# Kernel optimization log

Hardware: AMD Instinct MI355X
Metric: run time of the kernel (lower is better)

Reference implementation:

```python
import jax, jax.numpy as jnp
import numpy as np

BS, NS, NCP, NH, C, HID, R = 8, 2048, 8, 8, 128, 128, 128


def rotation_6d_to_matrix(d6):
    a1, a2 = d6[..., :3], d6[..., 3:]
    b1 = a1 / jnp.linalg.norm(a1, axis=-1, keepdims=True)
    b2 = a2 - jnp.sum(b1 * a2, axis=-1, keepdims=True) * b1
    b2 = b2 / jnp.linalg.norm(b2, axis=-1, keepdims=True)
    b3 = jnp.cross(b1, b2)
    return jnp.stack([b1, b2, b3], axis=-2)  # (..., 3, 3), rows b1,b2,b3


def _sample_plane(plane, uv):
    # plane: (B,C,R,R); uv: (B,N,2) in [0,1]; uv[...,0]->width, uv[...,1]->height
    Rr = plane.shape[-1]
    x = jnp.clip(uv[..., 0], 0.0, 1.0) * (Rr - 1)
    y = jnp.clip(uv[..., 1], 0.0, 1.0) * (Rr - 1)
    x0 = jnp.floor(x); y0 = jnp.floor(y)
    wx = x - x0; wy = y - y0
    x0i = x0.astype(jnp.int32); y0i = y0.astype(jnp.int32)
    x1i = jnp.minimum(x0i + 1, Rr - 1); y1i = jnp.minimum(y0i + 1, Rr - 1)
    gb = jax.vmap(lambda p, yi, xi: p[:, yi, xi])  # per-batch gather -> (C,N)
    f00 = gb(plane, y0i, x0i); f01 = gb(plane, y0i, x1i)
    f10 = gb(plane, y1i, x0i); f11 = gb(plane, y1i, x1i)
    wx = wx[:, None, :]; wy = wy[:, None, :]
    f = f00 * (1 - wx) * (1 - wy) + f01 * wx * (1 - wy) + f10 * (1 - wx) * wy + f11 * wx * wy
    return jnp.transpose(f, (0, 2, 1))  # (B,N,C)


def triplane_sample(p, pxz, pxy, pyz):
    # p: (B,N,3) in [0,1]^3; sum of bilinear samples from the three planes
    return (_sample_plane(pxz, p[..., jnp.array([0, 2])])
            + _sample_plane(pxy, p[..., jnp.array([0, 1])])
            + _sample_plane(pyz, p[..., jnp.array([1, 2])]))


def setup_inputs() -> dict:
    key = jax.random.key(0)
    ks = jax.random.split(key, 10)
    s = 1.0 / np.sqrt(C)
    return {
        "query_pos": jax.random.uniform(ks[0], (BS, NS, 9), dtype=jnp.float32),
        "plane_xz": jax.random.normal(ks[1], (BS, C, R, R), dtype=jnp.float32),
        "plane_xy": jax.random.normal(ks[2], (BS, C, R, R), dtype=jnp.float32),
        "plane_yz": jax.random.normal(ks[3], (BS, C, R, R), dtype=jnp.float32),
        "control_points": jax.random.normal(ks[4], (NCP, 3), dtype=jnp.float32) * 0.05,
        "W_v": jax.random.normal(ks[5], (C, HID), dtype=jnp.float32) * s,
        "b_v": jnp.zeros((HID,), jnp.float32),
        "W_w": jax.random.normal(ks[6], (C, NCP * NH), dtype=jnp.float32) * s,
        "b_w": jnp.zeros((NCP * NH,), jnp.float32),
        "W_o": jax.random.normal(ks[7], (HID, C), dtype=jnp.float32) * s,
        "b_o": jnp.zeros((C,), jnp.float32),
    }


def reference(query_pos, plane_xz, plane_xy, plane_yz, control_points,
              W_v, b_v, W_w, b_w, W_o, b_o):
    bs, ns, _ = query_pos.shape
    q_ori = query_pos[..., 3:]
    q_pos = query_pos[..., :3]
    feature = triplane_sample(q_pos, plane_xz, plane_xy, plane_yz)  # (bs,ns,C)
    rot = rotation_6d_to_matrix(q_ori)  # (bs,ns,3,3)
    # rotate control points: einsum('bnpd,bngd->bngp') with cp broadcast over (bs,ns)
    cp = jnp.einsum('bnpd,gd->bngp', rot, control_points)  # (bs,ns,ncp,3)
    anchor = q_pos[:, :, None, :] + cp  # (bs,ns,ncp,3)
    sf = triplane_sample(anchor.reshape(bs, ns * NCP, 3), plane_xz, plane_xy, plane_yz)
    sf = sf.reshape(bs * ns, NCP, C)  # head dim in torch code is a pure repeat
    feat = feature.reshape(bs * ns, C)
    w = (feat @ W_w + b_w).reshape(bs * ns, NCP, NH)  # (B,ncp,heads)
    vbase = sf @ W_v + b_v  # (B,ncp,hid); identical across repeated head dim
    # torch: (v * weights).sum((1,2)) with v_t[b,i,j,k]=vbase[b,j,k], w[b,i,j]
    out = jnp.einsum('bjk,bij->bk', vbase, w)  # (B,hid)
    out = out @ W_o + b_o
    out = out + feat
    return out.reshape(bs, ns, -1)
```

## Files before the change

### kernel.cpp

```cpp
#include <hip/hip_runtime.h>
#include <hip/hip_fp16.h>
#include <math.h>

constexpr int BS  = 8;
constexpr int NS  = 2048;
constexpr int NCP = 8;
constexpr int NH  = 8;
constexpr int C   = 128;
constexpr int HID = 128;
constexpr int RR  = 128;

constexpr int QPB = 8;
constexpr int VEC = 4;

constexpr int NPOS = RR * RR;
constexpr size_t PLE = (size_t)BS * NPOS * C;

constexpr int NBLK_T = 1536;
constexpr int QPOS   = 512;
constexpr int SPOS   = 256;
constexpr int LROWH  = 260;

constexpr int NBINS  = 4096;
constexpr int NQ     = BS * NS;

using f4v = __attribute__((ext_vector_type(4))) float;

struct F4 { float x, y, z, w; };
__device__ __forceinline__ F4 f4add(F4 a, F4 b) {
    return F4{a.x + b.x, a.y + b.y, a.z + b.z, a.w + b.w};
}
__device__ __forceinline__ F4 f4fma(F4 acc, float s, F4 v) {
    return F4{fmaf(s, v.x, acc.x), fmaf(s, v.y, acc.y),
              fmaf(s, v.z, acc.z), fmaf(s, v.w, acc.w)};
}

__global__ __launch_bounds__(256) void trans_prep_k(
    const float* __restrict__ pxz, const float* __restrict__ pxy,
    const float* __restrict__ pyz, __half* __restrict__ dst,
    const float* __restrict__ Wv, const float* __restrict__ bv,
    const float* __restrict__ Ww, const float* __restrict__ bw,
    const float* __restrict__ Wo,
    float* __restrict__ Wf, float* __restrict__ bf,
    float* __restrict__ Ww2, float* __restrict__ bw2,
    unsigned* __restrict__ hist)
{
    __shared__ __half lh[64 * LROWH];

    const int bid = blockIdx.x;
    const int t   = threadIdx.x;

    if (bid >= NBLK_T + 130) {
        hist[(bid - (NBLK_T + 130)) * 256 + t] = 0u;
        return;
    }
    if (bid >= NBLK_T) {
        const int k = bid - NBLK_T;
        const int c = t;
        if (c >= 128) return;
        if (k < 128) {
            float acc = 0.f;
            #pragma unroll 8
            for (int j = 0; j < 128; ++j) acc += Wv[k * 128 + j] * Wo[j * 128 + c];
            Wf[k * 128 + c] = acc;
        } else if (k == 128) {
            float acc = 0.f;
            #pragma unroll 8
            for (int j = 0; j < 128; ++j) acc += bv[j] * Wo[j * 128 + c];
            bf[c] = acc;
        } else {
            float s[NH];
            #pragma unroll
            for (int h = 0; h < NH; ++h) s[h] = 0.f;
            #pragma unroll
            for (int i = 0; i < NCP; ++i)
                #pragma unroll
                for (int h = 0; h < NH; ++h) s[h] += Ww[c * (NCP * NH) + i * NH + h];
            #pragma unroll
            for (int h = 0; h < NH; ++h) Ww2[c * NH + h] = s[h];
            if (c < NH) {
                float tt = 0.f;
                #pragma unroll
                for (int i = 0; i < NCP; ++i) tt += bw[i * NH + c];
                bw2[c] = tt;
            }
        }
        return;
    }

    const int b    = bid & 7;
    const int rem  = bid >> 3;
    const int pl   = rem >> 6;
    const int r2   = rem & 63;
    const int cg   = r2 >> 5;
    const int q    = r2 & 31;
    const int ch0  = cg * 64;
    const int pos0 = q * QPOS;

    const float* src = (pl == 0 ? pxz : (pl == 1 ? pxy : pyz))
                       + (size_t)b * C * NPOS;
    __half* d = dst + (size_t)(pl * BS + b) * ((size_t)NPOS * C);

    const int g32  = t >> 5;
    const int l32  = t & 31;

    f4v v[16];
    #pragma unroll
    for (int i = 0; i < 16; ++i) {
        const int chL  = g32 * 8 + (i >> 1);
        const int posL = ((i & 1) << 7) + (l32 << 2);
        v[i] = __builtin_nontemporal_load(reinterpret_cast<const f4v*>(
                   src + (size_t)(ch0 + chL) * NPOS + pos0 + posL));
    }

    #pragma unroll
    for (int sc = 0; sc < 2; ++sc) {
        __syncthreads();

        #pragma unroll
        for (int i = 0; i < 16; ++i) {
            const int chL  = g32 * 8 + (i >> 1);
            const int posL = ((i & 1) << 7) + (l32 << 2);
            __half2 h0 = __floats2half2_rn(v[i][0], v[i][1]);
            __half2 h1 = __floats2half2_rn(v[i][2], v[i][3]);
            uint2 w;
            w.x = *reinterpret_cast<unsigned*>(&h0);
            w.y = *reinterpret_cast<unsigned*>(&h1);
            *reinterpret_cast<uint2*>(&lh[chL * LROWH + posL]) = w;
        }

        f4v nv[16];
        if (sc < 1) {
            #pragma unroll
            for (int i = 0; i < 16; ++i) {
                const int chL  = g32 * 8 + (i >> 1);
                const int posL = ((i & 1) << 7) + (l32 << 2);
                nv[i] = __builtin_nontemporal_load(reinterpret_cast<const f4v*>(
                            src + (size_t)(ch0 + chL) * NPOS + pos0
                                + (sc + 1) * SPOS + posL));
            }
        }
        __syncthreads();

        const int cbase = (t & 7) * 8;
        #pragma unroll
        for (int j = 0; j < 8; ++j) {
            const int p = 32 * j + (t >> 3);
            unsigned w[4];
            #pragma unroll
            for (int k = 0; k < 4; ++k) {
                const unsigned lo = *reinterpret_cast<const unsigned short*>(
                                        &lh[(cbase + 2 * k) * LROWH + p]);
                const unsigned hi = *reinterpret_cast<const unsigned short*>(
                                        &lh[(cbase + 2 * k + 1) * LROWH + p]);
                w[k] = lo | (hi << 16);
            }
            *reinterpret_cast<uint4*>(
                d + (size_t)(pos0 + sc * SPOS + p) * C + ch0 + cbase) =
                make_uint4(w[0], w[1], w[2], w[3]);
        }

        #pragma unroll
        for (int i = 0; i < 16; ++i) v[i] = nv[i];
    }
}

__device__ __forceinline__ int bin_of(const float* qp) {
    int bx = min((int)(fminf(fmaxf(qp[0], 0.f), 1.f) * 8.f), 7);
    int by = min((int)(fminf(fmaxf(qp[1], 0.f), 1.f) * 8.f), 7);
    int bz = min((int)(fminf(fmaxf(qp[2], 0.f), 1.f) * 8.f), 7);
    int m = 0;
    #pragma unroll
    for (int i = 0; i < 3; ++i)
        m |= (((bx >> i) & 1) << (3 * i))
           | (((by >> i) & 1) << (3 * i + 1))
           | (((bz >> i) & 1) << (3 * i + 2));
    return m;
}

__global__ __launch_bounds__(256) void bin_count_k(
    const float* __restrict__ qpos, unsigned* __restrict__ hist,
    unsigned* __restrict__ binid)
{
    const int q = blockIdx.x * 256 + threadIdx.x;
    const float* qp = qpos + (size_t)q * 9;
    const int bin = ((q >> 11) << 9) | bin_of(qp);
    binid[q] = (unsigned)bin;
    atomicAdd(&hist[bin], 1u);
}

__global__ __launch_bounds__(1024) void scan_k(
    const unsigned* __restrict__ hist, unsigned* __restrict__ cursor)
{
    __shared__ unsigned s[1024];
    const int t = threadIdx.x;
    unsigned h[4];
    unsigned loc = 0;
    #pragma unroll
    for (int i = 0; i < 4; ++i) { h[i] = hist[t * 4 + i]; loc += h[i]; }
    s[t] = loc;
    __syncthreads();
    for (int off = 1; off < 1024; off <<= 1) {
        unsigned u = (t >= off) ? s[t - off] : 0u;
        __syncthreads();
        s[t] += u;
        __syncthreads();
    }
    unsigned excl = s[t] - loc;
    #pragma unroll
    for (int i = 0; i < 4; ++i) { cursor[t * 4 + i] = excl; excl += h[i]; }
}

__global__ __launch_bounds__(256) void scatter_k(
    const unsigned* __restrict__ binid, unsigned* __restrict__ cursor,
    unsigned* __restrict__ perm)
{
    const int q = blockIdx.x * 256 + threadIdx.x;
    const unsigned pos = atomicAdd(&cursor[binid[q]], 1u);
    perm[pos] = (unsigned)q;
}

__device__ __forceinline__ F4 samp(const __half* __restrict__ base, float u, float v)
{
    float x = fminf(fmaxf(u, 0.f), 1.f) * (float)(RR - 1);
    float y = fminf(fmaxf(v, 0.f), 1.f) * (float)(RR - 1);
    float x0f = floorf(x), y0f = floorf(y);
    float wx = x - x0f, wy = y - y0f;
    int x0 = (int)x0f, y0 = (int)y0f;
    int x1 = min(x0 + 1, RR - 1), y1 = min(y0 + 1, RR - 1);
    int r0 = y0 << 14, r1 = y1 << 14, cc0 = x0 << 7, cc1 = x1 << 7;
    int2 a00 = *reinterpret_cast<const int2*>(base + r0 + cc0);
    int2 a01 = *reinterpret_cast<const int2*>(base + r0 + cc1);
    int2 a10 = *reinterpret_cast<const int2*>(base + r1 + cc0);
    int2 a11 = *reinterpret_cast<const int2*>(base + r1 + cc1);

    float w00f = (1.f - wx) * (1.f - wy), w01f = wx * (1.f - wy);
    float w10f = (1.f - wx) * wy,         w11f = wx * wy;
    __half2 W00 = __float2half2_rn(w00f), W01 = __float2half2_rn(w01f);
    __half2 W10 = __float2half2_rn(w10f), W11 = __float2half2_rn(w11f);

    __half2 acc0 = __hmul2(*reinterpret_cast<__half2*>(&a00.x), W00);
    __half2 acc1 = __hmul2(*reinterpret_cast<__half2*>(&a00.y), W00);
    acc0 = __hfma2(*reinterpret_cast<__half2*>(&a01.x), W01, acc0);
    acc1 = __hfma2(*reinterpret_cast<__half2*>(&a01.y), W01, acc1);
    acc0 = __hfma2(*reinterpret_cast<__half2*>(&a10.x), W10, acc0);
    acc1 = __hfma2(*reinterpret_cast<__half2*>(&a10.y), W10, acc1);
    acc0 = __hfma2(*reinterpret_cast<__half2*>(&a11.x), W11, acc0);
    acc1 = __hfma2(*reinterpret_cast<__half2*>(&a11.y), W11, acc1);

    float2 f0 = __half22float2(acc0);
    float2 f1 = __half22float2(acc1);
    return F4{f0.x, f0.y, f1.x, f1.y};
}

__global__ __launch_bounds__(256) void attn_k(
    const float* __restrict__ qpos,
    const __half* __restrict__ planes,
    const float* __restrict__ cpts,
    const unsigned* __restrict__ perm,
    const float* __restrict__ Ww2, const float* __restrict__ bw2,
    const float* __restrict__ Wf,  const float* __restrict__ bf,
    const float* __restrict__ bo,
    float* __restrict__ out)
{
    const int nb   = gridDim.x;
    const int cpx  = nb >> 3;
    const int sbid = (blockIdx.x & 7) * cpx + (blockIdx.x >> 3);

    const int tid  = threadIdx.x;
    const int ql   = tid >> 5;
    const int lane = tid & 31;
    const int c4   = lane * VEC;
    const int q    = (int)perm[sbid * QPB + ql];
    const int b    = q >> 11;

    __shared__ unsigned sQ[QPB];
    if (lane == 0) sQ[ql] = (unsigned)q;

    const float* qp = qpos + (size_t)q * 9;
    const float px = qp[0], py = qp[1], pz = qp[2];
    const float a1x = qp[3], a1y = qp[4], a1z = qp[5];
    const float a2x = qp[6], a2y = qp[7], a2z = qp[8];

    float inv = 1.f / sqrtf(a1x * a1x + a1y * a1y + a1z * a1z);
    float b1x = a1x * inv, b1y = a1y * inv, b1z = a1z * inv;
    float dd  = b1x * a2x + b1y * a2y + b1z * a2z;
    float b2x = a2x - dd * b1x, b2y = a2y - dd * b1y, b2z = a2z - dd * b1z;
    inv = 1.f / sqrtf(b2x * b2x + b2y * b2y + b2z * b2z);
    b2x *= inv; b2y *= inv; b2z *= inv;
    float b3x = b1y * b2z - b1z * b2y;
    float b3y = b1z * b2x - b1x * b2z;
    float b3z = b1x * b2y - b1y * b2x;

    const __half* Pxz = planes + (size_t)b * ((size_t)NPOS * C) + c4;
    const __half* Pxy = Pxz + PLE;
    const __half* Pyz = Pxy + PLE;

    F4 feat = f4add(f4add(samp(Pxz, px, pz), samp(Pxy, px, py)), samp(Pyz, py, pz));

    float p[NH];
    #pragma unroll
    for (int h = 0; h < NH; ++h) p[h] = 0.f;
    {
        const float* wr = Ww2 + c4 * NH;
        const float fv[VEC] = {feat.x, feat.y, feat.z, feat.w};
        #pragma unroll
        for (int i = 0; i < VEC; ++i)
            #pragma unroll
            for (int h = 0; h < NH; ++h) p[h] += fv[i] * wr[i * NH + h];
    }
    #pragma unroll
    for (int off = 16; off >= 1; off >>= 1)
        #pragma unroll
        for (int h = 0; h < NH; ++h) p[h] += __shfl_xor(p[h], off);

    float ws[NH], Ssum = 0.f;
    #pragma unroll
    for (int h = 0; h < NH; ++h) { ws[h] = p[h] + bw2[h]; Ssum += ws[h]; }

    F4 comb = {0.f, 0.f, 0.f, 0.f};
    #pragma unroll 2
    for (int g = 0; g < NCP; ++g) {
        float cx = cpts[g * 3 + 0], cy = cpts[g * 3 + 1], cz = cpts[g * 3 + 2];
        float ax = px + b1x * cx + b1y * cy + b1z * cz;
        float ay = py + b2x * cx + b2y * cy + b2z * cz;
        float az = pz + b3x * cx + b3y * cy + b3z * cz;
        F4 s = f4add(f4add(samp(Pxz, ax, az), samp(Pxy, ax, ay)), samp(Pyz, ay, az));
        comb = f4fma(comb, ws[g], s);
    }

    __shared__ float sComb[QPB][C];
    __shared__ float sFeat[QPB][C];
    __shared__ float sSum[QPB];
    *reinterpret_cast<float4*>(&sComb[ql][c4]) = make_float4(comb.x, comb.y, comb.z, comb.w);
    *reinterpret_cast<float4*>(&sFeat[ql][c4]) = make_float4(feat.x, feat.y, feat.z, feat.w);
    if (lane == 0) sSum[ql] = Ssum;
    __syncthreads();

    const int c  = tid & 127;
    const int q0 = (tid >> 7) * 4;
    float acc[4];
    const float bfc = bf[c], boc = bo[c];
    #pragma unroll
    for (int j = 0; j < 4; ++j)
        acc[j] = sSum[q0 + j] * bfc + boc + sFeat[q0 + j][c];
    #pragma unroll 4
    for (int k = 0; k < C; ++k) {
        float wf = Wf[k * C + c];
        #pragma unroll
        for (int j = 0; j < 4; ++j) acc[j] += sComb[q0 + j][k] * wf;
    }
    #pragma unroll
    for (int j = 0; j < 4; ++j)
        out[(size_t)sQ[q0 + j] * C + c] = acc[j];
}

extern "C" void kernel_launch(void* const* d_in, const int* in_sizes, int n_in,
                              void* d_out, int out_size, void* d_ws, size_t ws_size,
                              hipStream_t stream)
{
    const float* qpos = (const float*)d_in[0];
    const float* pxz  = (const float*)d_in[1];
    const float* pxy  = (const float*)d_in[2];
    const float* pyz  = (const float*)d_in[3];
    const float* cpts = (const float*)d_in[4];
    const float* Wv   = (const float*)d_in[5];
    const float* bv   = (const float*)d_in[6];
    const float* Ww   = (const float*)d_in[7];
    const float* bw   = (const float*)d_in[8];
    const float* Wo   = (const float*)d_in[9];
    const float* bo   = (const float*)d_in[10];
    float* out = (float*)d_out;

    __half* plh = (__half*)d_ws;
    float*  wsf = (float*)((char*)d_ws + 3 * PLE * sizeof(__half));
    float* Wf  = wsf;
    float* bf  = Wf + C * HID;
    float* Ww2 = bf + C;
    float* bw2 = Ww2 + C * NH;
    unsigned* hist   = (unsigned*)(bw2 + NH);
    unsigned* cursor = hist + NBINS;
    unsigned* binid  = cursor + NBINS;
    unsigned* perm   = binid + NQ;

    hipLaunchKernelGGL(trans_prep_k, dim3(NBLK_T + 130 + 16), dim3(256), 0, stream,
                       pxz, pxy, pyz, plh, Wv, bv, Ww, bw, Wo, Wf, bf, Ww2, bw2,
                       hist);
    hipLaunchKernelGGL(bin_count_k, dim3(NQ / 256), dim3(256), 0, stream,
                       qpos, hist, binid);
    hipLaunchKernelGGL(scan_k, dim3(1), dim3(1024), 0, stream, hist, cursor);
    hipLaunchKernelGGL(scatter_k, dim3(NQ / 256), dim3(256), 0, stream,
                       binid, cursor, perm);
    hipLaunchKernelGGL(attn_k, dim3(NQ / QPB), dim3(256), 0, stream,
                       qpos, plh, cpts, perm, Ww2, bw2, Wf, bf, bo, out);
}
```

Measured before the change: 116.3 us.

## Widen per-lane sampling to 8 channels with fp16 accumulation and double queries per block

Each query is now handled by 16 lanes that each fetch 8 half channels per corner with 16-byte loads, so each block covers 16 queries. The three-plane sums and the control-point weighted combination are accumulated in packed fp16 instead of fp32. In the final projection each thread computes 8 queries, so every Wf load is reused twice as often. The aim is fewer, wider gather instructions and less load and arithmetic overhead per channel, at the cost of more fp16 rounding error and higher register pressure.

```diff
diff --git a/kernel.cpp b/kernel.cpp
--- a/kernel.cpp
+++ b/kernel.cpp
@@ -10,8 +10,9 @@
 constexpr int HID = 128;
 constexpr int RR  = 128;
 
-constexpr int QPB = 8;
-constexpr int VEC = 4;
+constexpr int QPB = 16;
+constexpr int LPQ = 16;
+constexpr int VEC = 8;
 
 constexpr int NPOS = RR * RR;
 constexpr size_t PLE = (size_t)BS * NPOS * C;
@@ -26,13 +27,12 @@
 
 using f4v = __attribute__((ext_vector_type(4))) float;
 
-struct F4 { float x, y, z, w; };
-__device__ __forceinline__ F4 f4add(F4 a, F4 b) {
-    return F4{a.x + b.x, a.y + b.y, a.z + b.z, a.w + b.w};
-}
-__device__ __forceinline__ F4 f4fma(F4 acc, float s, F4 v) {
-    return F4{fmaf(s, v.x, acc.x), fmaf(s, v.y, acc.y),
-              fmaf(s, v.z, acc.z), fmaf(s, v.w, acc.w)};
+struct H8 { __half2 h[4]; };
+__device__ __forceinline__ H8 h8add(H8 a, H8 b) {
+    H8 r;
+    #pragma unroll
+    for (int j = 0; j < 4; ++j) r.h[j] = __hadd2(a.h[j], b.h[j]);
+    return r;
 }
 
 __global__ __launch_bounds__(256) void trans_prep_k(
@@ -220,7 +220,8 @@
     perm[pos] = (unsigned)q;
 }
 
-__device__ __forceinline__ F4 samp(const __half* __restrict__ base, float u, float v)
+__device__ __forceinline__ H8 samp8(const __half* __restrict__ base,
+                                    float u, float v)
 {
     float x = fminf(fmaxf(u, 0.f), 1.f) * (float)(RR - 1);
     float y = fminf(fmaxf(v, 0.f), 1.f) * (float)(RR - 1);
@@ -229,28 +230,31 @@
     int x0 = (int)x0f, y0 = (int)y0f;
     int x1 = min(x0 + 1, RR - 1), y1 = min(y0 + 1, RR - 1);
     int r0 = y0 << 14, r1 = y1 << 14, cc0 = x0 << 7, cc1 = x1 << 7;
-    int2 a00 = *reinterpret_cast<const int2*>(base + r0 + cc0);
-    int2 a01 = *reinterpret_cast<const int2*>(base + r0 + cc1);
-    int2 a10 = *reinterpret_cast<const int2*>(base + r1 + cc0);
-    int2 a11 = *reinterpret_cast<const int2*>(base + r1 + cc1);
+    int4 a00 = *reinterpret_cast<const int4*>(base + r0 + cc0);
+    int4 a01 = *reinterpret_cast<const int4*>(base + r0 + cc1);
+    int4 a10 = *reinterpret_cast<const int4*>(base + r1 + cc0);
+    int4 a11 = *reinterpret_cast<const int4*>(base + r1 + cc1);
 
     float w00f = (1.f - wx) * (1.f - wy), w01f = wx * (1.f - wy);
     float w10f = (1.f - wx) * wy,         w11f = wx * wy;
     __half2 W00 = __float2half2_rn(w00f), W01 = __float2half2_rn(w01f);
     __half2 W10 = __float2half2_rn(w10f), W11 = __float2half2_rn(w11f);
 
-    __half2 acc0 = __hmul2(*reinterpret_cast<__half2*>(&a00.x), W00);
-    __half2 acc1 = __hmul2(*reinterpret_cast<__half2*>(&a00.y), W00);
-    acc0 = __hfma2(*reinterpret_cast<__half2*>(&a01.x), W01, acc0);
-    acc1 = __hfma2(*reinterpret_cast<__half2*>(&a01.y), W01, acc1);
-    acc0 = __hfma2(*reinterpret_cast<__half2*>(&a10.x), W10, acc0);
-    acc1 = __hfma2(*reinterpret_cast<__half2*>(&a10.y), W10, acc1);
-    acc0 = __hfma2(*reinterpret_cast<__half2*>(&a11.x), W11, acc0);
-    acc1 = __hfma2(*reinterpret_cast<__half2*>(&a11.y), W11, acc1);
-
-    float2 f0 = __half22float2(acc0);
-    float2 f1 = __half22float2(acc1);
-    return F4{f0.x, f0.y, f1.x, f1.y};
+    const __half2* p00 = reinterpret_cast<const __half2*>(&a00);
+    const __half2* p01 = reinterpret_cast<const __half2*>(&a01);
+    const __half2* p10 = reinterpret_cast<const __half2*>(&a10);
+    const __half2* p11 = reinterpret_cast<const __half2*>(&a11);
+
+    H8 r;
+    #pragma unroll
+    for (int j = 0; j < 4; ++j) {
+        __half2 acc = __hmul2(p00[j], W00);
+        acc = __hfma2(p01[j], W01, acc);
+        acc = __hfma2(p10[j], W10, acc);
+        acc = __hfma2(p11[j], W11, acc);
+        r.h[j] = acc;
+    }
+    return r;
 }
 
 __global__ __launch_bounds__(256) void attn_k(
@@ -268,9 +272,9 @@
     const int sbid = (blockIdx.x & 7) * cpx + (blockIdx.x >> 3);
 
     const int tid  = threadIdx.x;
-    const int ql   = tid >> 5;
-    const int lane = tid & 31;
-    const int c4   = lane * VEC;
+    const int ql   = tid >> 4;
+    const int lane = tid & 15;
+    const int c8   = lane * VEC;
     const int q    = (int)perm[sbid * QPB + ql];
     const int b    = q >> 11;
 
@@ -292,66 +296,94 @@
     float b3y = b1z * b2x - b1x * b2z;
     float b3z = b1x * b2y - b1y * b2x;
 
-    const __half* Pxz = planes + (size_t)b * ((size_t)NPOS * C) + c4;
+    const __half* Pxz = planes + (size_t)b * ((size_t)NPOS * C) + c8;
     const __half* Pxy = Pxz + PLE;
     const __half* Pyz = Pxy + PLE;
 
-    F4 feat = f4add(f4add(samp(Pxz, px, pz), samp(Pxy, px, py)), samp(Pyz, py, pz));
+    H8 fh = h8add(h8add(samp8(Pxz, px, pz), samp8(Pxy, px, py)),
+                  samp8(Pyz, py, pz));
+    float feat[VEC];
+    #pragma unroll
+    for (int j = 0; j < 4; ++j) {
+        float2 f = __half22float2(fh.h[j]);
+        feat[2 * j] = f.x; feat[2 * j + 1] = f.y;
+    }
 
     float p[NH];
     #pragma unroll
     for (int h = 0; h < NH; ++h) p[h] = 0.f;
     {
-        const float* wr = Ww2 + c4 * NH;
-        const float fv[VEC] = {feat.x, feat.y, feat.z, feat.w};
+        const float* wr = Ww2 + c8 * NH;
         #pragma unroll
         for (int i = 0; i < VEC; ++i)
             #pragma unroll
-            for (int h = 0; h < NH; ++h) p[h] += fv[i] * wr[i * NH + h];
-    }
-    #pragma unroll
-    for (int off = 16; off >= 1; off >>= 1)
+            for (int h = 0; h < NH; ++h) p[h] += feat[i] * wr[i * NH + h];
+    }
+    #pragma unroll
+    for (int off = 8; off >= 1; off >>= 1)
         #pragma unroll
         for (int h = 0; h < NH; ++h) p[h] += __shfl_xor(p[h], off);
 
     float ws[NH], Ssum = 0.f;
     #pragma unroll
     for (int h = 0; h < NH; ++h) { ws[h] = p[h] + bw2[h]; Ssum += ws[h]; }
-
-    F4 comb = {0.f, 0.f, 0.f, 0.f};
+    __half2 wsh[NCP];
+    #pragma unroll
+    for (int g = 0; g < NCP; ++g) wsh[g] = __float2half2_rn(ws[g]);
+
+    __half2 comb_h[4];
+    #pragma unroll
+    for (int j = 0; j < 4; ++j) comb_h[j] = __float2half2_rn(0.f);
     #pragma unroll 2
     for (int g = 0; g < NCP; ++g) {
         float cx = cpts[g * 3 + 0], cy = cpts[g * 3 + 1], cz = cpts[g * 3 + 2];
         float ax = px + b1x * cx + b1y * cy + b1z * cz;
         float ay = py + b2x * cx + b2y * cy + b2z * cz;
         float az = pz + b3x * cx + b3y * cy + b3z * cz;
-        F4 s = f4add(f4add(samp(Pxz, ax, az), samp(Pxy, ax, ay)), samp(Pyz, ay, az));
-        comb = f4fma(comb, ws[g], s);
+        H8 s = h8add(h8add(samp8(Pxz, ax, az), samp8(Pxy, ax, ay)),
+                     samp8(Pyz, ay, az));
+        #pragma unroll
+        for (int j = 0; j < 4; ++j)
+            comb_h[j] = __hfma2(s.h[j], wsh[g], comb_h[j]);
     }
 
     __shared__ float sComb[QPB][C];
     __shared__ float sFeat[QPB][C];
     __shared__ float sSum[QPB];
-    *reinterpret_cast<float4*>(&sComb[ql][c4]) = make_float4(comb.x, comb.y, comb.z, comb.w);
-    *reinterpret_cast<float4*>(&sFeat[ql][c4]) = make_float4(feat.x, feat.y, feat.z, feat.w);
+    {
+        float cf[VEC];
+        #pragma unroll
+        for (int j = 0; j < 4; ++j) {
+            float2 f = __half22float2(comb_h[j]);
+            cf[2 * j] = f.x; cf[2 * j + 1] = f.y;
+        }
+        *reinterpret_cast<float4*>(&sComb[ql][c8])     =
+            make_float4(cf[0], cf[1], cf[2], cf[3]);
+        *reinterpret_cast<float4*>(&sComb[ql][c8 + 4]) =
+            make_float4(cf[4], cf[5], cf[6], cf[7]);
+        *reinterpret_cast<float4*>(&sFeat[ql][c8])     =
+            make_float4(feat[0], feat[1], feat[2], feat[3]);
+        *reinterpret_cast<float4*>(&sFeat[ql][c8 + 4]) =
+            make_float4(feat[4], feat[5], feat[6], feat[7]);
+    }
     if (lane == 0) sSum[ql] = Ssum;
     __syncthreads();
 
     const int c  = tid & 127;
-    const int q0 = (tid >> 7) * 4;
-    float acc[4];
+    const int q0 = (tid >> 7) * 8;
+    float acc[8];
     const float bfc = bf[c], boc = bo[c];
     #pragma unroll
-    for (int j = 0; j < 4; ++j)
+    for (int j = 0; j < 8; ++j)
         acc[j] = sSum[q0 + j] * bfc + boc + sFeat[q0 + j][c];
     #pragma unroll 4
     for (int k = 0; k < C; ++k) {
         float wf = Wf[k * C + c];
         #pragma unroll
-        for (int j = 0; j < 4; ++j) acc[j] += sComb[q0 + j][k] * wf;
-    }
-    #pragma unroll
-    for (int j = 0; j < 4; ++j)
+        for (int j = 0; j < 8; ++j) acc[j] += sComb[q0 + j][k] * wf;
+    }
+    #pragma unroll
+    for (int j = 0; j < 8; ++j)
         out[(size_t)sQ[q0 + j] * C + c] = acc[j];
 }
 
```

Result: slower. 121.0 us (+4.0%).

## Fuse query binning histogram, scan and scatter into one single-block kernel

Applied to the files above, without the earlier changes.

Replaces the three-kernel counting sort (global histogram, single-block scan, atomic scatter) and the hist-zeroing blocks in the prep kernel with one 1024-thread kernel that keeps the histogram in shared memory. This drops two kernel launches and the global atomics and round trips through binid, hist and cursor. In exchange, all 16K queries are binned by a single workgroup on one CU, which serialises that work and runs ahead of the plane transpose kernel in the stream.

```diff
diff --git a/kernel.cpp b/kernel.cpp
--- a/kernel.cpp
+++ b/kernel.cpp
@@ -42,18 +42,13 @@
     const float* __restrict__ Ww, const float* __restrict__ bw,
     const float* __restrict__ Wo,
     float* __restrict__ Wf, float* __restrict__ bf,
-    float* __restrict__ Ww2, float* __restrict__ bw2,
-    unsigned* __restrict__ hist)
+    float* __restrict__ Ww2, float* __restrict__ bw2)
 {
     __shared__ __half lh[64 * LROWH];
 
     const int bid = blockIdx.x;
     const int t   = threadIdx.x;
 
-    if (bid >= NBLK_T + 130) {
-        hist[(bid - (NBLK_T + 130)) * 256 + t] = 0u;
-        return;
-    }
     if (bid >= NBLK_T) {
         const int k = bid - NBLK_T;
         const int c = t;
@@ -165,59 +160,63 @@
     }
 }
 
-__device__ __forceinline__ int bin_of(const float* qp) {
-    int bx = min((int)(fminf(fmaxf(qp[0], 0.f), 1.f) * 8.f), 7);
-    int by = min((int)(fminf(fmaxf(qp[1], 0.f), 1.f) * 8.f), 7);
-    int bz = min((int)(fminf(fmaxf(qp[2], 0.f), 1.f) * 8.f), 7);
-    int m = 0;
-    #pragma unroll
-    for (int i = 0; i < 3; ++i)
-        m |= (((bx >> i) & 1) << (3 * i))
-           | (((by >> i) & 1) << (3 * i + 1))
-           | (((bz >> i) & 1) << (3 * i + 2));
-    return m;
-}
-
-__global__ __launch_bounds__(256) void bin_count_k(
-    const float* __restrict__ qpos, unsigned* __restrict__ hist,
-    unsigned* __restrict__ binid)
-{
-    const int q = blockIdx.x * 256 + threadIdx.x;
-    const float* qp = qpos + (size_t)q * 9;
-    const int bin = ((q >> 11) << 9) | bin_of(qp);
-    binid[q] = (unsigned)bin;
-    atomicAdd(&hist[bin], 1u);
-}
-
-__global__ __launch_bounds__(1024) void scan_k(
-    const unsigned* __restrict__ hist, unsigned* __restrict__ cursor)
-{
-    __shared__ unsigned s[1024];
+__global__ __launch_bounds__(1024) void bin_all_k(
+    const float* __restrict__ qpos, unsigned* __restrict__ perm)
+{
+    __shared__ unsigned hist[NBINS];
+    __shared__ unsigned part[1024];
+
     const int t = threadIdx.x;
-    unsigned h[4];
-    unsigned loc = 0;
+    #pragma unroll
+    for (int i = 0; i < 4; ++i) hist[t * 4 + i] = 0u;
+
+    float psx[16], psy[16], psz[16];
+    #pragma unroll
+    for (int i = 0; i < 16; ++i) {
+        const float* qp = qpos + (size_t)(i * 1024 + t) * 9;
+        psx[i] = qp[0]; psy[i] = qp[1]; psz[i] = qp[2];
+    }
+    __syncthreads();
+
+    int bins[16];
+    #pragma unroll
+    for (int i = 0; i < 16; ++i) {
+        const int q = i * 1024 + t;
+        int bx = min((int)(fminf(fmaxf(psx[i], 0.f), 1.f) * 8.f), 7);
+        int by = min((int)(fminf(fmaxf(psy[i], 0.f), 1.f) * 8.f), 7);
+        int bz = min((int)(fminf(fmaxf(psz[i], 0.f), 1.f) * 8.f), 7);
+        int m = 0;
+        #pragma unroll
+        for (int j = 0; j < 3; ++j)
+            m |= (((bx >> j) & 1) << (3 * j))
+               | (((by >> j) & 1) << (3 * j + 1))
+               | (((bz >> j) & 1) << (3 * j + 2));
+        bins[i] = ((q >> 11) << 9) | m;
+        atomicAdd(&hist[bins[i]], 1u);
+    }
+    __syncthreads();
+
+    unsigned h[4], loc = 0;
     #pragma unroll
     for (int i = 0; i < 4; ++i) { h[i] = hist[t * 4 + i]; loc += h[i]; }
-    s[t] = loc;
+    part[t] = loc;
     __syncthreads();
     for (int off = 1; off < 1024; off <<= 1) {
-        unsigned u = (t >= off) ? s[t - off] : 0u;
+        unsigned u = (t >= off) ? part[t - off] : 0u;
         __syncthreads();
-        s[t] += u;
+        part[t] += u;
         __syncthreads();
     }
-    unsigned excl = s[t] - loc;
-    #pragma unroll
-    for (int i = 0; i < 4; ++i) { cursor[t * 4 + i] = excl; excl += h[i]; }
-}
-
-__global__ __launch_bounds__(256) void scatter_k(
-    const unsigned* __restrict__ binid, unsigned* __restrict__ cursor,
-    unsigned* __restrict__ perm)
-{
-    const int q = blockIdx.x * 256 + threadIdx.x;
-    const unsigned pos = atomicAdd(&cursor[binid[q]], 1u);
-    perm[pos] = (unsigned)q;
+    unsigned excl = part[t] - loc;
+    #pragma unroll
+    for (int i = 0; i < 4; ++i) { hist[t * 4 + i] = excl; excl += h[i]; }
+    __syncthreads();
+
+    #pragma unroll
+    for (int i = 0; i < 16; ++i) {
+        const unsigned pos = atomicAdd(&hist[bins[i]], 1u);
+        perm[pos] = (unsigned)(i * 1024 + t);
+    }
 }
 
 __device__ __forceinline__ F4 samp(const __half* __restrict__ base, float u, float v)
@@ -378,19 +377,11 @@
     float* bf  = Wf + C * HID;
     float* Ww2 = bf + C;
     float* bw2 = Ww2 + C * NH;
-    unsigned* hist   = (unsigned*)(bw2 + NH);
-    unsigned* cursor = hist + NBINS;
-    unsigned* binid  = cursor + NBINS;
-    unsigned* perm   = binid + NQ;
-
-    hipLaunchKernelGGL(trans_prep_k, dim3(NBLK_T + 130 + 16), dim3(256), 0, stream,
-                       pxz, pxy, pyz, plh, Wv, bv, Ww, bw, Wo, Wf, bf, Ww2, bw2,
-                       hist);
-    hipLaunchKernelGGL(bin_count_k, dim3(NQ / 256), dim3(256), 0, stream,
-                       qpos, hist, binid);
-    hipLaunchKernelGGL(scan_k, dim3(1), dim3(1024), 0, stream, hist, cursor);
-    hipLaunchKernelGGL(scatter_k, dim3(NQ / 256), dim3(256), 0, stream,
-                       binid, cursor, perm);
+    unsigned* perm = (unsigned*)(bw2 + NH);
+
+    hipLaunchKernelGGL(bin_all_k, dim3(1), dim3(1024), 0, stream, qpos, perm);
+    hipLaunchKernelGGL(trans_prep_k, dim3(NBLK_T + 130), dim3(256), 0, stream,
+                       pxz, pxy, pyz, plh, Wv, bv, Ww, bw, Wo, Wf, bf, Ww2, bw2);
     hipLaunchKernelGGL(attn_k, dim3(NQ / QPB), dim3(256), 0, stream,
                        qpos, plh, cpts, perm, Ww2, bw2, Wf, bf, bo, out);
 }
```

New measurement: 125.2 us. +7.6%, slower.
